# Optimization experiments

Hardware: AMD Instinct MI355X
Metric: run time of the kernel (lower is better)

Reference implementation:

```python
import jax, jax.numpy as jnp
import numpy as np

B, T_ENC, D_IN = 8, 512, 512
T_DEC, ODIM = 150, 80
D_RNN, PRE, ATTN, LOC, K = 1024, 256, 128, 32, 31
ZONEOUT = 0.1


def setup_inputs() -> dict:
    key = jax.random.key(0)
    ks = jax.random.split(key, 24)
    s = 0.02
    n = jax.random.normal
    inp = {
        "memory": n(ks[0], (B, T_ENC, D_IN), jnp.float32),
        "memory_length": jax.random.randint(ks[1], (B,), 256, T_ENC + 1, jnp.int32),
        "targets": n(ks[2], (B, T_DEC, ODIM), jnp.float32),
        # location-sensitive attention params
        "W_mem": n(ks[3], (ATTN, D_IN), jnp.float32) * s,
        "W_q": n(ks[4], (ATTN, D_RNN), jnp.float32) * s,
        "W_loc": n(ks[5], (ATTN, LOC), jnp.float32) * s,
        "loc_filters": n(ks[6], (LOC, 1, K), jnp.float32) * s,
        "attn_v": n(ks[7], (ATTN,), jnp.float32) * s,
        "attn_b": jnp.zeros((ATTN,), jnp.float32),
        # prenet (80 -> 256 -> 256)
        "pre_W1": n(ks[8], (PRE, ODIM), jnp.float32) * s,
        "pre_b1": jnp.zeros((PRE,), jnp.float32),
        "pre_W2": n(ks[9], (PRE, PRE), jnp.float32) * s,
        "pre_b2": jnp.zeros((PRE,), jnp.float32),
        # LSTM layer 0: input = D_IN + PRE
        "Wi0": n(ks[10], (4 * D_RNN, D_IN + PRE), jnp.float32) * s,
        "Wh0": n(ks[11], (4 * D_RNN, D_RNN), jnp.float32) * s,
        "bl0": jnp.zeros((4 * D_RNN,), jnp.float32),
        # LSTM layer 1
        "Wi1": n(ks[12], (4 * D_RNN, D_RNN), jnp.float32) * s,
        "Wh1": n(ks[13], (4 * D_RNN, D_RNN), jnp.float32) * s,
        "bl1": jnp.zeros((4 * D_RNN,), jnp.float32),
        # projections from zcs = [h_last, att_c] of width D_RNN + D_IN
        "feat_W": n(ks[14], (ODIM, D_RNN + D_IN), jnp.float32) * s,
        "stop_W": n(ks[15], (1, D_RNN + D_IN), jnp.float32) * s,
        "stop_b": jnp.zeros((1,), jnp.float32),
    }
    return inp


def _lstm_cell(x, h, c, Wi, Wh, b):
    g = x @ Wi.T + h @ Wh.T + b
    i, f, gc, o = jnp.split(g, 4, axis=-1)  # torch LSTMCell gate order
    c_new = jax.nn.sigmoid(f) * c + jax.nn.sigmoid(i) * jnp.tanh(gc)
    h_new = jax.nn.sigmoid(o) * jnp.tanh(c_new)
    # zoneout (expected value / eval form)
    return (1.0 - ZONEOUT) * h_new + ZONEOUT * h, (1.0 - ZONEOUT) * c_new + ZONEOUT * c


def reference(memory, memory_length, targets, W_mem, W_q, W_loc, loc_filters,
              attn_v, attn_b, pre_W1, pre_b1, pre_W2, pre_b2,
              Wi0, Wh0, bl0, Wi1, Wh1, bl1, feat_W, stop_W, stop_b):
    b, t_enc, _ = memory.shape
    proc_mem = jnp.einsum('btd,ad->bta', memory, W_mem)           # [B,T,ATTN]
    mask = jnp.arange(t_enc)[None, :] < memory_length[:, None]    # [B,T]

    def step(carry, prev_out):
        h0, c0, h1, c1, att_cum = carry
        # location features: conv over cumulative attention weights
        f = jax.lax.conv_general_dilated(att_cum[:, None, :], loc_filters,
                                         (1,), 'SAME')            # [B,LOC,T]
        loc = jnp.einsum('bct,ac->bta', f, W_loc)                  # [B,T,ATTN]
        q = (h0 @ W_q.T)[:, None, :]                               # [B,1,ATTN]
        e = jnp.einsum('a,bta->bt', attn_v,
                       jnp.tanh(proc_mem + loc + q + attn_b))      # [B,T]
        att_w = jax.nn.softmax(jnp.where(mask, e, -1e9), axis=-1)
        att_c = jnp.einsum('bt,btd->bd', att_w, memory)            # [B,D_IN]
        # prenet on previous output (dropout off: deterministic reference)
        p = jax.nn.relu(prev_out @ pre_W1.T + pre_b1)
        p = jax.nn.relu(p @ pre_W2.T + pre_b2)
        x = jnp.concatenate([att_c, p], axis=1)                    # [B,D_IN+PRE]
        h0, c0 = _lstm_cell(x, h0, c0, Wi0, Wh0, bl0)
        h1, c1 = _lstm_cell(h0, h1, c1, Wi1, Wh1, bl1)
        zcs = jnp.concatenate([h1, att_c], axis=1)                 # use_concate=True
        out = zcs @ feat_W.T                                       # [B,ODIM]
        stop = zcs @ stop_W.T + stop_b                             # [B,1]
        return (h0, c0, h1, c1, att_cum + att_w), (out, stop, att_w)

    z = jnp.zeros((b, D_RNN), memory.dtype)
    init = (z, z, z, z, jnp.zeros((b, t_enc), memory.dtype))
    # teacher forcing: prev_out at step t is targets[t-1], zeros at t=0
    prev_outs = jnp.concatenate(
        [jnp.zeros((b, 1, ODIM), targets.dtype), targets[:, :-1]], axis=1)
    _, (outs, stops, att_ws) = jax.lax.scan(step, init,
                                            jnp.swapaxes(prev_outs, 0, 1))
    before_outs = jnp.swapaxes(outs, 0, 1)         # [B,T_dec,ODIM]
    stops = jnp.swapaxes(stops, 0, 1)[..., 0]      # [B,T_dec]
    att_ws = jnp.swapaxes(att_ws, 0, 1)            # [B,T_dec,T_enc]
    return before_outs, stops, att_ws
```

## Files before the change

### kernel.cpp

```cpp
#include <hip/hip_runtime.h>
#include <hip/hip_fp16.h>
#include <cstdint>
#include <cstddef>


#define NB 256
#define NT 512

#define Bz   8
#define TE   512
#define DINz 512
#define TDz  150
#define ODz  80
#define DRz  1024
#define PREz 256
#define ATz  128
#define LOCz 32
#define KFz  31

#define OF_P    0
#define OF_PM   307200
#define OF_Q    831488
#define OF_U    832512
#define OF_CUM  836608
#define OF_ATTC 840704
#define OF_S    848896
#define OF_INVS 848912
#define OF_H0   848928
#define OF_C0   857120
#define OF_H1   865312
#define OF_C1   873504
#define OF_GH0  881696
#define OF_GH1  914464
#define OF_BAR  947232

#define OFF_X0   0
#define OFF_X1   2048
#define OFF_EX   4096
#define OFF_EXG  4352
#define OFF_CW   4608
#define OFF_QS   4736
#define OFF_PART 4864
#define OFF_UU   5376
#define OFF_F    5632
#define OFF_V    9600
#define OFF_WA   9728
#define OFF_WB   22016
#define OFF_WG1  4608
#define OFF_WG2  20992
#define SM_TOTF  38400

#define AG __HIP_MEMORY_SCOPE_AGENT

__device__ __forceinline__ float ldg_sc1(const float* p){
  return __hip_atomic_load(p, __ATOMIC_RELAXED, AG);
}
__device__ __forceinline__ void stg_sc1(float* p, float v){
  __hip_atomic_store(p, v, __ATOMIC_RELAXED, AG);
}
__device__ __forceinline__ float4 ldg4_sc1(const float* p){
  float4 r; r.x=ldg_sc1(p); r.y=ldg_sc1(p+1); r.z=ldg_sc1(p+2); r.w=ldg_sc1(p+3);
  return r;
}
__device__ __forceinline__ float fsig_(float x){ return 1.f/(1.f + __expf(-x)); }
__device__ __forceinline__ float ftanh_(float x){
  x = fminf(10.f, fmaxf(-10.f, x));
  float e = __expf(2.f*x);
  return (e - 1.f) / (e + 1.f);
}

__device__ __forceinline__ void grid_barrier(int* bar){
  asm volatile("s_waitcnt vmcnt(0) lgkmcnt(0)" ::: "memory");
  __syncthreads();
  if (threadIdx.x == 0){
    const int lf = blockIdx.x >> 4;
    int* leaf  = bar + (lf << 5);
    int* root  = bar + 512;
    int* ep    = bar + 1024 + (lf << 5);
    int g = __hip_atomic_load(ep, __ATOMIC_RELAXED, AG);
    int lo = __hip_atomic_fetch_add(leaf, 1, __ATOMIC_RELAXED, AG);
    if ((lo & 15) == 15){
      int ro = __hip_atomic_fetch_add(root, 1, __ATOMIC_RELAXED, AG);
      if ((ro & 15) == 15){
        #pragma unroll
        for (int i=0;i<16;++i)
          __hip_atomic_store(bar + 1024 + (i<<5), g + 1, __ATOMIC_RELAXED, AG);
      }
    }
    while (__hip_atomic_load(ep, __ATOMIC_RELAXED, AG) == g)
      __builtin_amdgcn_s_sleep(1);
  }
  __syncthreads();
}
__device__ __forceinline__ void grid_barrier_heavy(int* bar){
  asm volatile("s_waitcnt vmcnt(0) lgkmcnt(0)" ::: "memory");
  __syncthreads();
  if (threadIdx.x == 0){
    __builtin_amdgcn_fence(__ATOMIC_RELEASE, "agent");
    const int lf = blockIdx.x >> 4;
    int* leaf  = bar + (lf << 5);
    int* root  = bar + 512;
    int* ep    = bar + 1024 + (lf << 5);
    int g = __hip_atomic_load(ep, __ATOMIC_RELAXED, AG);
    int lo = __hip_atomic_fetch_add(leaf, 1, __ATOMIC_RELAXED, AG);
    if ((lo & 15) == 15){
      int ro = __hip_atomic_fetch_add(root, 1, __ATOMIC_RELAXED, AG);
      if ((ro & 15) == 15){
        #pragma unroll
        for (int i=0;i<16;++i)
          __hip_atomic_store(bar + 1024 + (i<<5), g + 1, __ATOMIC_RELAXED, AG);
      }
    }
    while (__hip_atomic_load(ep, __ATOMIC_RELAXED, AG) == g)
      __builtin_amdgcn_s_sleep(1);
    __builtin_amdgcn_fence(__ATOMIC_ACQUIRE, "agent");
  }
  __syncthreads();
}

template<int K, bool GM>
__device__ void load_wtile(float* dstf, const float* __restrict__ W, int base){
  __half* dst = (__half*)dstf;
  constexpr int KV = K >> 2;
  constexpr int NV = 32 * KV;
  for (int idx = threadIdx.x; idx < NV; idx += NT){
    int r = idx / KV;
    int c = (idx - r*KV) << 2;
    int grow = GM ? (((r>>3)<<10) + base + (r&7)) : (base + r);
    float4 w = *(const float4*)(W + (size_t)grow*K + c);
    __half* d = dst + (size_t)r*K + c;
    d[0] = __float2half_rn(w.x);
    d[1] = __float2half_rn(w.y);
    d[2] = __float2half_rn(w.z);
    d[3] = __float2half_rn(w.w);
  }
}

__device__ __forceinline__ float reduce_dot(float* sm, float (&acc)[2][8]){
  const int tid = threadIdx.x;
  const int s = tid & 31, pos = tid >> 5;
  #pragma unroll
  for (int i=0;i<2;++i){
    #pragma unroll
    for (int b=0;b<8;++b){
      float v = acc[i][b];
      v += __shfl_xor(v, 16, 64);
      v += __shfl_xor(v,  8, 64);
      v += __shfl_xor(v,  4, 64);
      v += __shfl_xor(v,  2, 64);
      v += __shfl_xor(v,  1, 64);
      acc[i][b] = v;
    }
  }
  if (s == 0){
    #pragma unroll
    for (int i=0;i<2;++i)
      #pragma unroll
      for (int b=0;b<8;++b)
        sm[OFF_EX + ((((pos<<1)+i)<<3) | b)] = acc[i][b];
  }
  __syncthreads();
  return (tid < 256) ? sm[OFF_EX + tid] : 0.f;
}

template<int K, int XMODE>
__device__ float gemm32x8_lds(float* sm, const __half* __restrict__ wlds,
                              const float* __restrict__ xsrc,
                              const float* __restrict__ attc_cur,
                              const float* __restrict__ S_cur,
                              const float* __restrict__ Pt)
{
  constexpr int NCH = K >> 8;
  const int tid = threadIdx.x;
  const int s = tid & 31, pos = tid >> 5;
  float acc[2][8];
  #pragma unroll
  for (int i=0;i<2;++i)
    #pragma unroll
    for (int b=0;b<8;++b) acc[i][b] = 0.f;

  const int xb = tid >> 6, xcol = (tid & 63) << 2;
  float4 xreg[NCH];
  if constexpr (XMODE == 0){
    #pragma unroll
    for (int ch=0; ch<NCH; ++ch)
      xreg[ch] = ldg4_sc1(xsrc + (size_t)xb*K + (ch<<8) + xcol);
  } else {
    float xsc = 1.f / ldg_sc1(S_cur + xb);
    #pragma unroll
    for (int ch=0; ch<2; ++ch){
      float4 v = ldg4_sc1(attc_cur + (xb<<9) + (ch<<8) + xcol);
      v.x*=xsc; v.y*=xsc; v.z*=xsc; v.w*=xsc;
      xreg[ch] = v;
    }
    xreg[2] = *(const float4*)(Pt + (xb<<8) + xcol);
  }
  *(float4*)&sm[OFF_X0 + (xb<<8) + xcol] = xreg[0];
  __syncthreads();
  #pragma unroll
  for (int ch=0; ch<NCH; ++ch){
    if (ch+1 < NCH)
      *(float4*)&sm[(((ch+1)&1) ? OFF_X1 : OFF_X0) + (xb<<8) + xcol] = xreg[(ch+1 < NCH) ? ch+1 : 0];
    const float* xbase = &sm[((ch&1) ? OFF_X1 : OFF_X0)];
    const __half* wch = wlds + (ch<<8);
    #pragma unroll
    for (int j=0;j<2;++j){
      const int k = (j<<7) + (s<<2);
      float4 xv[8];
      #pragma unroll
      for (int b=0;b<8;++b) xv[b] = *(const float4*)&xbase[(b<<8) + k];
      #pragma unroll
      for (int i=0;i<2;++i){
        const int row = (pos<<1) + i;
        uint2 w2 = *(const uint2*)&wch[(size_t)row*K + k];
        __half2 ha = *reinterpret_cast<const __half2*>(&w2.x);
        __half2 hb = *reinterpret_cast<const __half2*>(&w2.y);
        float2 fa = __half22float2(ha);
        float2 fb = __half22float2(hb);
        #pragma unroll
        for (int b=0;b<8;++b){
          acc[i][b] = fmaf(fa.x, xv[b].x, acc[i][b]);
          acc[i][b] = fmaf(fa.y, xv[b].y, acc[i][b]);
          acc[i][b] = fmaf(fb.x, xv[b].z, acc[i][b]);
          acc[i][b] = fmaf(fb.y, xv[b].w, acc[i][b]);
        }
      }
    }
    __syncthreads();
  }
  return reduce_dot(sm, acc);
}

__device__ float gemm32x8_gw(float* sm, const float* __restrict__ W, int rowbase,
                             const float* __restrict__ xsrc)
{
  const int tid = threadIdx.x;
  const int s = tid & 31, pos = tid >> 5;
  float acc[2][8];
  #pragma unroll
  for (int i=0;i<2;++i)
    #pragma unroll
    for (int b=0;b<8;++b) acc[i][b] = 0.f;
  const int xb = tid >> 6, xcol = (tid & 63) << 2;
  float4 xreg[4];
  #pragma unroll
  for (int ch=0; ch<4; ++ch)
    xreg[ch] = ldg4_sc1(xsrc + (size_t)xb*1024 + (ch<<8) + xcol);
  const float* w0 = W + (size_t)(rowbase + (pos<<1))*1024 + (s<<2);
  *(float4*)&sm[OFF_X0 + (xb<<8) + xcol] = xreg[0];
  __syncthreads();
  #pragma unroll
  for (int ch=0; ch<4; ++ch){
    float4 wr[2][2];
    #pragma unroll
    for (int j=0;j<2;++j)
      #pragma unroll
      for (int i=0;i<2;++i)
        wr[j][i] = *(const float4*)(w0 + (size_t)i*1024 + (ch<<8) + (j<<7));
    if (ch+1 < 4)
      *(float4*)&sm[(((ch+1)&1) ? OFF_X1 : OFF_X0) + (xb<<8) + xcol] = xreg[(ch+1<4)?ch+1:0];
    const float* xbase = &sm[((ch&1) ? OFF_X1 : OFF_X0)];
    #pragma unroll
    for (int j=0;j<2;++j){
      const int k = (j<<7) + (s<<2);
      float4 xv[8];
      #pragma unroll
      for (int b=0;b<8;++b) xv[b] = *(const float4*)&xbase[(b<<8) + k];
      #pragma unroll
      for (int i=0;i<2;++i){
        float4 wv = wr[j][i];
        #pragma unroll
        for (int b=0;b<8;++b){
          acc[i][b] = fmaf(wv.x, xv[b].x, acc[i][b]);
          acc[i][b] = fmaf(wv.y, xv[b].y, acc[i][b]);
          acc[i][b] = fmaf(wv.z, xv[b].z, acc[i][b]);
          acc[i][b] = fmaf(wv.w, xv[b].w, acc[i][b]);
        }
      }
    }
    __syncthreads();
  }
  return reduce_dot(sm, acc);
}

__device__ __forceinline__ float prefetch_gh(const float* gh, int u0){
  const int tid = threadIdx.x;
  if (tid >= 256) return 0.f;
  int row32 = tid >> 3, b = tid & 7;
  int gate = row32 >> 3, ul = row32 & 7;
  return ldg_sc1(&gh[(((gate<<10) + u0 + ul)<<3) + b]);
}
__device__ __forceinline__ float prefetch_h(const float* h, int u0){
  const int tid = threadIdx.x;
  if (tid >= 64) return 0.f;
  return ldg_sc1(&h[((tid&7)<<10) + u0 + (tid>>3)]);
}

__device__ void lstm_epilogue(float* sm, float dot, float ghb,
                              const float* __restrict__ bias, float hold,
                              float* __restrict__ h, float* __restrict__ c, int u0)
{
  const int tid = threadIdx.x;
  if (tid < 256){
    int row32 = tid >> 3;
    int gate = row32 >> 3, ul = row32 & 7;
    sm[OFF_EXG + tid] = dot + bias[(gate<<10) + u0 + ul] + ghb;
  }
  __syncthreads();
  if (tid < 64){
    float gi = sm[OFF_EXG + tid];
    float gf = sm[OFF_EXG + 64 + tid];
    float gg = sm[OFF_EXG + 128 + tid];
    float go = sm[OFF_EXG + 192 + tid];
    int ul2 = tid >> 3, b2 = tid & 7;
    int hi = (b2<<10) + u0 + ul2;
    float co = c[hi];
    float cn = fsig_(gf)*co + fsig_(gi)*ftanh_(gg);
    float hn = fsig_(go)*ftanh_(cn);
    c[hi] = 0.9f*cn + 0.1f*co;
    stg_sc1(&h[hi], 0.9f*hn + 0.1f*hold);
  }
}

__device__ void outstop_wave(int rr, int tp, int par,
    const float* __restrict__ feat_W, const float* __restrict__ stop_W,
    const float* __restrict__ stop_b, const float* __restrict__ h1,
    const float* __restrict__ attc, const float* __restrict__ iSw,
    float* __restrict__ d_out)
{
  if (rr >= 648) return;
  int b = rr / 81, r = rr - 81*b;
  int lane = threadIdx.x & 63;
  const float4* Wr = (const float4*)((r < 80) ? (feat_W + (size_t)r*1536) : stop_W);
  float inv = ldg_sc1(iSw + (par<<3) + b);
  float acc = 0.f, acc2 = 0.f;
  #pragma unroll
  for (int j=0;j<4;++j){
    int p = lane + (j<<6);
    float4 w = Wr[p], x = ldg4_sc1(h1 + (b<<10) + (p<<2));
    acc = fmaf(w.x,x.x, fmaf(w.y,x.y, fmaf(w.z,x.z, fmaf(w.w,x.w, acc))));
  }
  #pragma unroll
  for (int j=4;j<6;++j){
    int p = lane + (j<<6);
    float4 w = Wr[p], x = ldg4_sc1(attc + (par<<12) + (b<<9) + ((p-256)<<2));
    acc2 = fmaf(w.x,x.x, fmaf(w.y,x.y, fmaf(w.z,x.z, fmaf(w.w,x.w, acc2))));
  }
  acc += acc2 * inv;
  acc += __shfl_down(acc, 32, 64);
  acc += __shfl_down(acc, 16, 64);
  acc += __shfl_down(acc,  8, 64);
  acc += __shfl_down(acc,  4, 64);
  acc += __shfl_down(acc,  2, 64);
  acc += __shfl_down(acc,  1, 64);
  if (lane == 0){
    if (r < 80) d_out[((size_t)b*TDz + tp)*ODz + r] = acc;
    else        d_out[96000 + (size_t)b*TDz + tp] = acc + stop_b[0];
  }
}

extern "C" __global__ void __launch_bounds__(NT, 2) dec_kernel(
  const float* __restrict__ memory, const int* __restrict__ mlen, const float* __restrict__ targets,
  const float* __restrict__ W_mem, const float* __restrict__ W_q, const float* __restrict__ W_loc,
  const float* __restrict__ loc_f, const float* __restrict__ attn_v, const float* __restrict__ attn_b,
  const float* __restrict__ pre_W1, const float* __restrict__ pre_b1,
  const float* __restrict__ pre_W2, const float* __restrict__ pre_b2,
  const float* __restrict__ Wi0, const float* __restrict__ Wh0, const float* __restrict__ bl0,
  const float* __restrict__ Wi1, const float* __restrict__ Wh1, const float* __restrict__ bl1,
  const float* __restrict__ feat_W, const float* __restrict__ stop_W, const float* __restrict__ stop_b,
  float* __restrict__ d_out, float* __restrict__ ws)
{
  __shared__ float sm[SM_TOTF];
  const int blk = blockIdx.x, tid = threadIdx.x;

  float* Pw   = ws + OF_P;
  float* pmT  = ws + OF_PM;
  float* qw   = ws + OF_Q;
  float* uw   = ws + OF_U;
  float* cum  = ws + OF_CUM;
  float* attc = ws + OF_ATTC;
  float* Sw   = ws + OF_S;
  float* iSw  = ws + OF_INVS;
  float* h0 = ws + OF_H0; float* c0 = ws + OF_C0;
  float* h1 = ws + OF_H1; float* c1 = ws + OF_C1;
  float* gh0 = ws + OF_GH0; float* gh1 = ws + OF_GH1;
  int* bar = (int*)(ws + OF_BAR);

  const bool is_attn = (blk < 64);
  const int ab  = blk >> 3;
  const int ai0 = (blk & 7) << 6;
  const int il  = tid & 63;
  const int ag  = tid >> 6;

  {
    const int gs = NB*NT;
    const int gid = blk*NT + tid;
    for (int i = gid; i < 98304; i += gs) h0[i] = 0.f;
    for (int i = gid; i < 1024;  i += gs) qw[i]  = 0.f;
    for (int i = gid; i < 4096;  i += gs) cum[i] = 0.f;
    for (int i = gid; i < 8192;  i += gs) attc[i] = 0.f;
    if (gid < 32) Sw[gid] = 0.f;

    if (blk < 124){
      load_wtile<768, true >(&sm[OFF_WA], Wi0, blk<<3);
      load_wtile<1024,false>(&sm[OFF_WB], Wh0, blk<<5);
    } else if (blk < 128){
      load_wtile<768, true >(&sm[OFF_WA], Wi0, blk<<3);
      load_wtile<1024,false>(&sm[OFF_WB], W_q, (blk-124)<<5);
    } else {
      load_wtile<1024,false>(&sm[OFF_WG1], Wh1, (blk-128)<<5);
      load_wtile<1024,true >(&sm[OFF_WG2], Wi1, (blk-128)<<3);
    }

    if (is_attn){
      float pacc[16];
      #pragma unroll
      for (int j=0;j<16;++j) pacc[j] = 0.f;
      for (int dc=0; dc<4; ++dc){
        for (int idx = tid; idx < 8192; idx += NT){
          int r = idx >> 7, d = idx & 127;
          sm[r*129 + d] = memory[(size_t)((ab<<9)+ai0+r)*DINz + (dc<<7) + d];
        }
        __syncthreads();
        #pragma unroll
        for (int j=0;j<16;++j){
          int a = (ag<<4) + j;
          const float* wr = W_mem + (size_t)a*DINz + (dc<<7);
          const float* mr = &sm[il*129];
          float acc = 0.f;
          for (int d=0; d<128; d+=4){
            acc = fmaf(mr[d  ], wr[d  ], acc);
            acc = fmaf(mr[d+1], wr[d+1], acc);
            acc = fmaf(mr[d+2], wr[d+2], acc);
            acc = fmaf(mr[d+3], wr[d+3], acc);
          }
          pacc[j] += acc;
        }
        __syncthreads();
      }
      #pragma unroll
      for (int j=0;j<16;++j){
        int a = (ag<<4) + j;
        pmT[((size_t)blk<<13) + (a<<6) + il] = pacc[j] + attn_b[a];
      }
      for (int idx = tid; idx < ATz*KFz; idx += NT){
        int a = idx / KFz, k = idx - a*KFz;
        float s2 = 0.f;
        #pragma unroll
        for (int c2=0;c2<LOCz;++c2) s2 = fmaf(W_loc[(a<<5)+c2], loc_f[c2*KFz+k], s2);
        sm[OFF_F + idx] = s2;
      }
      if (tid < 128) sm[OFF_V + tid] = attn_v[tid];
      __syncthreads();
    }

    const int th = tid >> 8, t2 = tid & 255, base = th << 9;
    for (int it=0; it<3; ++it){
      int pp = (blk<<1) + th + (it<<9);
      bool act = pp < 1200;
      if (act && t2 < ODz){
        int tt = pp >> 3, bb = pp & 7;
        sm[base + t2] = (tt==0) ? 0.f : targets[((size_t)bb*TDz + (tt-1))*ODz + t2];
      }
      __syncthreads();
      if (act){
        float a1 = pre_b1[t2];
        for (int k=0;k<ODz;++k) a1 = fmaf(pre_W1[t2*ODz+k], sm[base+k], a1);
        sm[base + 128 + t2] = fmaxf(a1, 0.f);
      }
      __syncthreads();
      if (act){
        float a2 = pre_b2[t2];
        for (int k=0;k<PREz;++k) a2 = fmaf(pre_W2[(t2<<8)+k], sm[base+128+k], a2);
        Pw[((size_t)pp<<8) + t2] = fmaxf(a2, 0.f);
      }
      __syncthreads();
    }
  }
  grid_barrier_heavy(bar);

  for (int t = 0; t < TDz; ++t){
    const int cur = t & 1, prv = cur ^ 1;

    if (is_attn){
      if (tid < 94){
        int gi = ai0 - 15 + tid;
        sm[OFF_CW + tid] = (gi >= 0 && gi < TE) ? ldg_sc1(&cum[(ab<<9)+gi]) : 0.f;
      }
      if (tid < 128) sm[OFF_QS + tid] = ldg_sc1(&qw[(tid<<3) + ab]);
      __syncthreads();
      float part = 0.f;
      #pragma unroll
      for (int j=0;j<16;++j){
        int a = (ag<<4) + j;
        const float* fb = &sm[OFF_F + a*KFz];
        float conv = 0.f;
        #pragma unroll
        for (int k=0;k<KFz;++k) conv = fmaf(fb[k], sm[OFF_CW + il + k], conv);
        float pv = pmT[((size_t)blk<<13) + (a<<6) + il];
        part = fmaf(sm[OFF_V + a], ftanh_(pv + sm[OFF_QS + a] + conv), part);
      }
      sm[OFF_PART + (il<<3) + ag] = part;
      __syncthreads();
      if (tid < 64){
        float e = 0.f;
        #pragma unroll
        for (int k=0;k<8;++k) e += sm[OFF_PART + (tid<<3) + k];
        int gi = ai0 + tid;
        float uu = (gi < mlen[ab]) ? __expf(e) : 0.f;
        stg_sc1(&uw[(ab<<9)+gi], uu);
        sm[OFF_UU + tid] = uu;
      }
      __syncthreads();
      if (tid == 0){
        float ssum = 0.f;
        #pragma unroll
        for (int k=0;k<64;++k) ssum += sm[OFF_UU + k];
        atomicAdd(&Sw[(cur<<3)+ab], ssum);
      }
      {
        float acc = 0.f;
        const float* mrow = memory + (size_t)((ab<<9)+ai0)*DINz + tid;
        #pragma unroll 8
        for (int i=0;i<64;++i)
          acc = fmaf(sm[OFF_UU + i], mrow[(size_t)i*DINz], acc);
        atomicAdd(&attc[(cur<<12) + (ab<<9) + tid], acc);
      }
    } else if (blk < 68){
      const int tile = 124 + (blk - 64);
      float dot = gemm32x8_gw(sm, Wh0, tile<<5, h0);
      if (tid < 256) stg_sc1(&gh0[(tile<<8) + tid], dot);
    } else if (blk >= 128){
      const int tile = blk - 128;
      float dot = gemm32x8_lds<1024,0>(sm, (const __half*)&sm[OFF_WG1], h1,
                                       nullptr, nullptr, nullptr);
      if (tid < 256) stg_sc1(&gh1[(tile<<8) + tid], dot);
    }
    grid_barrier(bar);

    if (blk < 128){
      const int u0 = blk << 3;
      float ghb  = prefetch_gh(gh0, u0);
      float hold = prefetch_h(h0, u0);
      float dot = gemm32x8_lds<768,1>(sm, (const __half*)&sm[OFF_WA], nullptr,
                                      attc + (cur<<12), Sw + (cur<<3),
                                      Pw + ((size_t)t<<11));
      lstm_epilogue(sm, dot, ghb, bl0, hold, h0, c0, u0);
    } else if (blk < 136){
      const int b = blk - 128;
      float Sv = __hip_atomic_load(&Sw[(cur<<3)+b], __ATOMIC_RELAXED, AG);
      float inv = 1.f / Sv;
      if (tid == 0) stg_sc1(&iSw[(cur<<3)+b], inv);
      for (int i = tid; i < TE; i += NT){
        float u = ldg_sc1(&uw[(b<<9)+i]);
        float w = u * inv;
        d_out[97200 + ((size_t)b*TDz + t)*TE + i] = w;
        stg_sc1(&cum[(b<<9)+i], ldg_sc1(&cum[(b<<9)+i]) + w);
      }
    } else if (blk < 217){
      if (t > 0)
        outstop_wave((blk-136)*8 + (tid>>6), t-1, prv,
                     feat_W, stop_W, stop_b, h1, attc, iSw, d_out);
    }
    grid_barrier(bar);

    if (blk < 124){
      float dot = gemm32x8_lds<1024,0>(sm, (const __half*)&sm[OFF_WB], h0,
                                       nullptr, nullptr, nullptr);
      if (tid < 256) stg_sc1(&gh0[(blk<<8) + tid], dot);
    } else if (blk < 128){
      const int rt = blk - 124;
      float dot = gemm32x8_lds<1024,0>(sm, (const __half*)&sm[OFF_WB], h0,
                                       nullptr, nullptr, nullptr);
      if (tid < 256) stg_sc1(&qw[(rt<<8) + tid], dot);
      const int zbase = (prv<<12) + (rt<<10);
      for (int i = tid; i < 1024; i += NT) stg_sc1(&attc[zbase + i], 0.f);
      if (rt == 0 && tid < 8) stg_sc1(&Sw[(prv<<3)+tid], 0.f);
    } else {
      const int u0 = (blk - 128) << 3;
      float ghb  = prefetch_gh(gh1, u0);
      float hold = prefetch_h(h1, u0);
      float dot = gemm32x8_lds<1024,0>(sm, (const __half*)&sm[OFF_WG2], h0,
                                       nullptr, nullptr, nullptr);
      lstm_epilogue(sm, dot, ghb, bl1, hold, h1, c1, u0);
    }
    grid_barrier(bar);
  }

  if (blk >= 136 && blk < 217)
    outstop_wave((blk-136)*8 + (tid>>6), TDz-1, 1,
                 feat_W, stop_W, stop_b, h1, attc, iSw, d_out);
}

extern "C" void kernel_launch(void* const* d_in, const int* in_sizes, int n_in,
                              void* d_out, int out_size, void* d_ws, size_t ws_size,
                              hipStream_t stream)
{
  (void)in_sizes; (void)n_in; (void)out_size; (void)ws_size;
  (void)hipMemsetAsync((char*)d_ws + (size_t)OF_BAR*4, 0, 6144, stream);
  dec_kernel<<<dim3(NB), dim3(NT), 0, stream>>>(
    (const float*)d_in[0],  (const int*)d_in[1],   (const float*)d_in[2],
    (const float*)d_in[3],  (const float*)d_in[4],  (const float*)d_in[5],
    (const float*)d_in[6],  (const float*)d_in[7],  (const float*)d_in[8],
    (const float*)d_in[9],  (const float*)d_in[10], (const float*)d_in[11], (const float*)d_in[12],
    (const float*)d_in[13], (const float*)d_in[14], (const float*)d_in[15],
    (const float*)d_in[16], (const float*)d_in[17], (const float*)d_in[18],
    (const float*)d_in[19], (const float*)d_in[20], (const float*)d_in[21],
    (float*)d_out, (float*)d_ws);
}
```

Baseline: 5.674 ms.

## Restructure decoder step into two-phase pipeline with fused LSTM weights in LDS

Reorganizes each decoder step from three grid barriers to two. Layer-1 LSTM now runs one step behind, in parallel with attention, using double-buffered h0/h1/qw/attc. Each block keeps concatenated input and recurrent fp16 weights in LDS, which removes the separate gh precompute pass and the global-weight GEMM. The query projection is folded into the layer-0 epilogue through atomics, and attention is spread over 128 blocks instead of 64. This adds atomic contention on qw and a larger LDS footprint, with occupancy dropping to one block per CU.

```diff
diff --git a/kernel.cpp b/kernel.cpp
--- a/kernel.cpp
+++ b/kernel.cpp
@@ -7,7 +7,6 @@
 #define NB 256
 #define NT 512
 
-#define Bz   8
 #define TE   512
 #define DINz 512
 #define TDz  150
@@ -18,37 +17,34 @@
 #define LOCz 32
 #define KFz  31
 
-#define OF_P    0
-#define OF_PM   307200
-#define OF_Q    831488
-#define OF_U    832512
-#define OF_CUM  836608
-#define OF_ATTC 840704
-#define OF_S    848896
-#define OF_INVS 848912
-#define OF_H0   848928
-#define OF_C0   857120
-#define OF_H1   865312
-#define OF_C1   873504
-#define OF_GH0  881696
-#define OF_GH1  914464
-#define OF_BAR  947232
+#define OF_P     0
+#define OF_PM    307200
+#define OF_Q     831488
+#define OF_U     833536
+#define OF_CUM   837632
+#define OF_ATTC  841728
+#define OF_ATTCN 849920
+#define OF_S     858112
+#define OF_H0    858128
+#define OF_C0    874512
+#define OF_H1    882704
+#define OF_C1    899088
+#define OF_BAR   907280
 
 #define OFF_X0   0
 #define OFF_X1   2048
 #define OFF_EX   4096
 #define OFF_EXG  4352
-#define OFF_CW   4608
-#define OFF_QS   4736
-#define OFF_PART 4864
-#define OFF_UU   5376
-#define OFF_F    5632
-#define OFF_V    9600
-#define OFF_WA   9728
-#define OFF_WB   22016
-#define OFF_WG1  4608
-#define OFF_WG2  20992
-#define SM_TOTF  38400
+#define OFF_HN   4608
+#define OFF_W    4672
+#define OFF_WQT  33344
+#define OFF_F    34368
+#define OFF_V    38336
+#define OFF_CW   38464
+#define OFF_QS   38528
+#define OFF_PART 38656
+#define OFF_UU   39168
+#define SM_TOTF  39200
 
 #define AG __HIP_MEMORY_SCOPE_AGENT
 
@@ -61,6 +57,9 @@
 __device__ __forceinline__ float4 ldg4_sc1(const float* p){
   float4 r; r.x=ldg_sc1(p); r.y=ldg_sc1(p+1); r.z=ldg_sc1(p+2); r.w=ldg_sc1(p+3);
   return r;
+}
+__device__ __forceinline__ void stg4_sc1(float* p, float4 v){
+  stg_sc1(p, v.x); stg_sc1(p+1, v.y); stg_sc1(p+2, v.z); stg_sc1(p+3, v.w);
 }
 __device__ __forceinline__ float fsig_(float x){ return 1.f/(1.f + __expf(-x)); }
 __device__ __forceinline__ float ftanh_(float x){
@@ -118,21 +117,32 @@
   __syncthreads();
 }
 
-template<int K, bool GM>
-__device__ void load_wtile(float* dstf, const float* __restrict__ W, int base){
-  __half* dst = (__half*)dstf;
-  constexpr int KV = K >> 2;
-  constexpr int NV = 32 * KV;
-  for (int idx = threadIdx.x; idx < NV; idx += NT){
-    int r = idx / KV;
-    int c = (idx - r*KV) << 2;
-    int grow = GM ? (((r>>3)<<10) + base + (r&7)) : (base + r);
-    float4 w = *(const float4*)(W + (size_t)grow*K + c);
-    __half* d = dst + (size_t)r*K + c;
-    d[0] = __float2half_rn(w.x);
-    d[1] = __float2half_rn(w.y);
-    d[2] = __float2half_rn(w.z);
-    d[3] = __float2half_rn(w.w);
+__device__ void load_wc0(float* smW, const float* __restrict__ Wi0,
+                         const float* __restrict__ Wh0, int u0){
+  __half* dst = (__half*)smW;
+  for (int idx = threadIdx.x; idx < 32*448; idx += NT){
+    int r = idx / 448, c4 = (idx - r*448) << 2;
+    int grow = ((r>>3)<<10) + u0 + (r&7);
+    const float* src = (c4 < 768) ? (Wi0 + (size_t)grow*768 + c4)
+                                  : (Wh0 + (size_t)grow*1024 + (c4-768));
+    float4 w = *(const float4*)src;
+    __half* d = dst + (size_t)r*1792 + c4;
+    d[0]=__float2half_rn(w.x); d[1]=__float2half_rn(w.y);
+    d[2]=__float2half_rn(w.z); d[3]=__float2half_rn(w.w);
+  }
+}
+__device__ void load_wc1(float* smW, const float* __restrict__ Wi1,
+                         const float* __restrict__ Wh1, int u0){
+  __half* dst = (__half*)smW;
+  for (int idx = threadIdx.x; idx < 32*512; idx += NT){
+    int r = idx >> 9, c4 = (idx & 511) << 2;
+    int grow = ((r>>3)<<10) + u0 + (r&7);
+    const float* src = (c4 < 1024) ? (Wi1 + (size_t)grow*1024 + c4)
+                                   : (Wh1 + (size_t)grow*1024 + (c4-1024));
+    float4 w = *(const float4*)src;
+    __half* d = dst + (size_t)r*2048 + c4;
+    d[0]=__float2half_rn(w.x); d[1]=__float2half_rn(w.y);
+    d[2]=__float2half_rn(w.z); d[3]=__float2half_rn(w.w);
   }
 }
 
@@ -163,44 +173,25 @@
   return (tid < 256) ? sm[OFF_EX + tid] : 0.f;
 }
 
-template<int K, int XMODE>
-__device__ float gemm32x8_lds(float* sm, const __half* __restrict__ wlds,
-                              const float* __restrict__ xsrc,
-                              const float* __restrict__ attc_cur,
-                              const float* __restrict__ S_cur,
-                              const float* __restrict__ Pt)
-{
-  constexpr int NCH = K >> 8;
+template<int NCH>
+__device__ float gemm_core(float* sm, const __half* __restrict__ wlds,
+                           float4 (&xreg)[NCH]){
   const int tid = threadIdx.x;
   const int s = tid & 31, pos = tid >> 5;
+  const int xb = tid >> 6, xcol = (tid & 63) << 2;
+  constexpr int K = NCH << 8;
   float acc[2][8];
   #pragma unroll
   for (int i=0;i<2;++i)
     #pragma unroll
     for (int b=0;b<8;++b) acc[i][b] = 0.f;
-
-  const int xb = tid >> 6, xcol = (tid & 63) << 2;
-  float4 xreg[NCH];
-  if constexpr (XMODE == 0){
-    #pragma unroll
-    for (int ch=0; ch<NCH; ++ch)
-      xreg[ch] = ldg4_sc1(xsrc + (size_t)xb*K + (ch<<8) + xcol);
-  } else {
-    float xsc = 1.f / ldg_sc1(S_cur + xb);
-    #pragma unroll
-    for (int ch=0; ch<2; ++ch){
-      float4 v = ldg4_sc1(attc_cur + (xb<<9) + (ch<<8) + xcol);
-      v.x*=xsc; v.y*=xsc; v.z*=xsc; v.w*=xsc;
-      xreg[ch] = v;
-    }
-    xreg[2] = *(const float4*)(Pt + (xb<<8) + xcol);
-  }
   *(float4*)&sm[OFF_X0 + (xb<<8) + xcol] = xreg[0];
   __syncthreads();
   #pragma unroll
   for (int ch=0; ch<NCH; ++ch){
     if (ch+1 < NCH)
-      *(float4*)&sm[(((ch+1)&1) ? OFF_X1 : OFF_X0) + (xb<<8) + xcol] = xreg[(ch+1 < NCH) ? ch+1 : 0];
+      *(float4*)&sm[(((ch+1)&1) ? OFF_X1 : OFF_X0) + (xb<<8) + xcol] =
+          xreg[(ch+1 < NCH) ? ch+1 : 0];
     const float* xbase = &sm[((ch&1) ? OFF_X1 : OFF_X0)];
     const __half* wch = wlds + (ch<<8);
     #pragma unroll
@@ -231,122 +222,34 @@
   return reduce_dot(sm, acc);
 }
 
-__device__ float gemm32x8_gw(float* sm, const float* __restrict__ W, int rowbase,
-                             const float* __restrict__ xsrc)
-{
-  const int tid = threadIdx.x;
-  const int s = tid & 31, pos = tid >> 5;
-  float acc[2][8];
-  #pragma unroll
-  for (int i=0;i<2;++i)
-    #pragma unroll
-    for (int b=0;b<8;++b) acc[i][b] = 0.f;
-  const int xb = tid >> 6, xcol = (tid & 63) << 2;
-  float4 xreg[4];
-  #pragma unroll
-  for (int ch=0; ch<4; ++ch)
-    xreg[ch] = ldg4_sc1(xsrc + (size_t)xb*1024 + (ch<<8) + xcol);
-  const float* w0 = W + (size_t)(rowbase + (pos<<1))*1024 + (s<<2);
-  *(float4*)&sm[OFF_X0 + (xb<<8) + xcol] = xreg[0];
-  __syncthreads();
-  #pragma unroll
-  for (int ch=0; ch<4; ++ch){
-    float4 wr[2][2];
-    #pragma unroll
-    for (int j=0;j<2;++j)
-      #pragma unroll
-      for (int i=0;i<2;++i)
-        wr[j][i] = *(const float4*)(w0 + (size_t)i*1024 + (ch<<8) + (j<<7));
-    if (ch+1 < 4)
-      *(float4*)&sm[(((ch+1)&1) ? OFF_X1 : OFF_X0) + (xb<<8) + xcol] = xreg[(ch+1<4)?ch+1:0];
-    const float* xbase = &sm[((ch&1) ? OFF_X1 : OFF_X0)];
-    #pragma unroll
-    for (int j=0;j<2;++j){
-      const int k = (j<<7) + (s<<2);
-      float4 xv[8];
-      #pragma unroll
-      for (int b=0;b<8;++b) xv[b] = *(const float4*)&xbase[(b<<8) + k];
-      #pragma unroll
-      for (int i=0;i<2;++i){
-        float4 wv = wr[j][i];
-        #pragma unroll
-        for (int b=0;b<8;++b){
-          acc[i][b] = fmaf(wv.x, xv[b].x, acc[i][b]);
-          acc[i][b] = fmaf(wv.y, xv[b].y, acc[i][b]);
-          acc[i][b] = fmaf(wv.z, xv[b].z, acc[i][b]);
-          acc[i][b] = fmaf(wv.w, xv[b].w, acc[i][b]);
-        }
-      }
-    }
-    __syncthreads();
-  }
-  return reduce_dot(sm, acc);
-}
-
-__device__ __forceinline__ float prefetch_gh(const float* gh, int u0){
-  const int tid = threadIdx.x;
-  if (tid >= 256) return 0.f;
-  int row32 = tid >> 3, b = tid & 7;
-  int gate = row32 >> 3, ul = row32 & 7;
-  return ldg_sc1(&gh[(((gate<<10) + u0 + ul)<<3) + b]);
-}
 __device__ __forceinline__ float prefetch_h(const float* h, int u0){
   const int tid = threadIdx.x;
   if (tid >= 64) return 0.f;
   return ldg_sc1(&h[((tid&7)<<10) + u0 + (tid>>3)]);
 }
 
-__device__ void lstm_epilogue(float* sm, float dot, float ghb,
-                              const float* __restrict__ bias, float hold,
-                              float* __restrict__ h, float* __restrict__ c, int u0)
-{
-  const int tid = threadIdx.x;
-  if (tid < 256){
-    int row32 = tid >> 3;
-    int gate = row32 >> 3, ul = row32 & 7;
-    sm[OFF_EXG + tid] = dot + bias[(gate<<10) + u0 + ul] + ghb;
-  }
-  __syncthreads();
-  if (tid < 64){
-    float gi = sm[OFF_EXG + tid];
-    float gf = sm[OFF_EXG + 64 + tid];
-    float gg = sm[OFF_EXG + 128 + tid];
-    float go = sm[OFF_EXG + 192 + tid];
-    int ul2 = tid >> 3, b2 = tid & 7;
-    int hi = (b2<<10) + u0 + ul2;
-    float co = c[hi];
-    float cn = fsig_(gf)*co + fsig_(gi)*ftanh_(gg);
-    float hn = fsig_(go)*ftanh_(cn);
-    c[hi] = 0.9f*cn + 0.1f*co;
-    stg_sc1(&h[hi], 0.9f*hn + 0.1f*hold);
-  }
-}
-
-__device__ void outstop_wave(int rr, int tp, int par,
+__device__ void outstop_wave(int rr, int tp,
     const float* __restrict__ feat_W, const float* __restrict__ stop_W,
-    const float* __restrict__ stop_b, const float* __restrict__ h1,
-    const float* __restrict__ attc, const float* __restrict__ iSw,
-    float* __restrict__ d_out)
+    const float* __restrict__ stop_b, const float* __restrict__ h1b,
+    const float* __restrict__ attcn, float* __restrict__ d_out)
 {
   if (rr >= 648) return;
   int b = rr / 81, r = rr - 81*b;
   int lane = threadIdx.x & 63;
   const float4* Wr = (const float4*)((r < 80) ? (feat_W + (size_t)r*1536) : stop_W);
-  float inv = ldg_sc1(iSw + (par<<3) + b);
-  float acc = 0.f, acc2 = 0.f;
+  float acc = 0.f;
   #pragma unroll
   for (int j=0;j<4;++j){
     int p = lane + (j<<6);
-    float4 w = Wr[p], x = ldg4_sc1(h1 + (b<<10) + (p<<2));
+    float4 w = Wr[p], x = ldg4_sc1(h1b + (b<<10) + (p<<2));
     acc = fmaf(w.x,x.x, fmaf(w.y,x.y, fmaf(w.z,x.z, fmaf(w.w,x.w, acc))));
   }
   #pragma unroll
   for (int j=4;j<6;++j){
     int p = lane + (j<<6);
-    float4 w = Wr[p], x = ldg4_sc1(attc + (par<<12) + (b<<9) + ((p-256)<<2));
-    acc2 = fmaf(w.x,x.x, fmaf(w.y,x.y, fmaf(w.z,x.z, fmaf(w.w,x.w, acc2))));
-  }
-  acc += acc2 * inv;
+    float4 w = Wr[p], x = ldg4_sc1(attcn + (b<<9) + ((p-256)<<2));
+    acc = fmaf(w.x,x.x, fmaf(w.y,x.y, fmaf(w.z,x.z, fmaf(w.w,x.w, acc))));
+  }
   acc += __shfl_down(acc, 32, 64);
   acc += __shfl_down(acc, 16, 64);
   acc += __shfl_down(acc,  8, 64);
@@ -359,7 +262,7 @@
   }
 }
 
-extern "C" __global__ void __launch_bounds__(NT, 2) dec_kernel(
+extern "C" __global__ void __launch_bounds__(NT, 1) dec_kernel(
   const float* __restrict__ memory, const int* __restrict__ mlen, const float* __restrict__ targets,
   const float* __restrict__ W_mem, const float* __restrict__ W_q, const float* __restrict__ W_loc,
   const float* __restrict__ loc_f, const float* __restrict__ attn_v, const float* __restrict__ attn_b,
@@ -379,52 +282,46 @@
   float* uw   = ws + OF_U;
   float* cum  = ws + OF_CUM;
   float* attc = ws + OF_ATTC;
+  float* attcn= ws + OF_ATTCN;
   float* Sw   = ws + OF_S;
-  float* iSw  = ws + OF_INVS;
   float* h0 = ws + OF_H0; float* c0 = ws + OF_C0;
   float* h1 = ws + OF_H1; float* c1 = ws + OF_C1;
-  float* gh0 = ws + OF_GH0; float* gh1 = ws + OF_GH1;
   int* bar = (int*)(ws + OF_BAR);
 
-  const bool is_attn = (blk < 64);
-  const int ab  = blk >> 3;
-  const int ai0 = (blk & 7) << 6;
-  const int il  = tid & 63;
-  const int ag  = tid >> 6;
+  const bool is_attn = (blk < 128);
+  const int ab  = blk >> 4;
+  const int ai0 = (blk & 15) << 5;
+  const int il  = tid & 31;
+  const int ag  = tid >> 5;
 
   {
     const int gs = NB*NT;
     const int gid = blk*NT + tid;
-    for (int i = gid; i < 98304; i += gs) h0[i] = 0.f;
-    for (int i = gid; i < 1024;  i += gs) qw[i]  = 0.f;
-    for (int i = gid; i < 4096;  i += gs) cum[i] = 0.f;
-    for (int i = gid; i < 8192;  i += gs) attc[i] = 0.f;
-    if (gid < 32) Sw[gid] = 0.f;
-
-    if (blk < 124){
-      load_wtile<768, true >(&sm[OFF_WA], Wi0, blk<<3);
-      load_wtile<1024,false>(&sm[OFF_WB], Wh0, blk<<5);
-    } else if (blk < 128){
-      load_wtile<768, true >(&sm[OFF_WA], Wi0, blk<<3);
-      load_wtile<1024,false>(&sm[OFF_WB], W_q, (blk-124)<<5);
+    for (int i = gid; i < (OF_BAR - OF_Q); i += gs) ws[OF_Q + i] = 0.f;
+
+    if (is_attn){
+      load_wc0(&sm[OFF_W], Wi0, Wh0, blk<<3);
+      for (int i = tid; i < 1024; i += NT){
+        int u = i >> 7, a = i & 127;
+        sm[OFF_WQT + i] = W_q[((size_t)a<<10) + (blk<<3) + u];
+      }
     } else {
-      load_wtile<1024,false>(&sm[OFF_WG1], Wh1, (blk-128)<<5);
-      load_wtile<1024,true >(&sm[OFF_WG2], Wi1, (blk-128)<<3);
+      load_wc1(&sm[OFF_W], Wi1, Wh1, (blk-128)<<3);
     }
 
     if (is_attn){
-      float pacc[16];
-      #pragma unroll
-      for (int j=0;j<16;++j) pacc[j] = 0.f;
+      float pacc[8];
+      #pragma unroll
+      for (int j=0;j<8;++j) pacc[j] = 0.f;
       for (int dc=0; dc<4; ++dc){
-        for (int idx = tid; idx < 8192; idx += NT){
+        for (int idx = tid; idx < 4096; idx += NT){
           int r = idx >> 7, d = idx & 127;
           sm[r*129 + d] = memory[(size_t)((ab<<9)+ai0+r)*DINz + (dc<<7) + d];
         }
         __syncthreads();
         #pragma unroll
-        for (int j=0;j<16;++j){
-          int a = (ag<<4) + j;
+        for (int j=0;j<8;++j){
+          int a = (ag<<3) + j;
           const float* wr = W_mem + (size_t)a*DINz + (dc<<7);
           const float* mr = &sm[il*129];
           float acc = 0.f;
@@ -439,9 +336,9 @@
         __syncthreads();
       }
       #pragma unroll
-      for (int j=0;j<16;++j){
-        int a = (ag<<4) + j;
-        pmT[((size_t)blk<<13) + (a<<6) + il] = pacc[j] + attn_b[a];
+      for (int j=0;j<8;++j){
+        int a = (ag<<3) + j;
+        pmT[((size_t)blk<<12) + (a<<5) + il] = pacc[j] + attn_b[a];
       }
       for (int idx = tid; idx < ATz*KFz; idx += NT){
         int a = idx / KFz, k = idx - a*KFz;
@@ -456,10 +353,10 @@
 
     const int th = tid >> 8, t2 = tid & 255, base = th << 9;
     for (int it=0; it<3; ++it){
-      int pp = (blk<<1) + th + (it<<9);
-      bool act = pp < 1200;
+      int pp2 = (blk<<1) + th + (it<<9);
+      bool act = pp2 < 1200;
       if (act && t2 < ODz){
-        int tt = pp >> 3, bb = pp & 7;
+        int tt = pp2 >> 3, bb = pp2 & 7;
         sm[base + t2] = (tt==0) ? 0.f : targets[((size_t)bb*TDz + (tt-1))*ODz + t2];
       }
       __syncthreads();
@@ -472,7 +369,7 @@
       if (act){
         float a2 = pre_b2[t2];
         for (int k=0;k<PREz;++k) a2 = fmaf(pre_W2[(t2<<8)+k], sm[base+128+k], a2);
-        Pw[((size_t)pp<<8) + t2] = fmaxf(a2, 0.f);
+        Pw[((size_t)pp2<<8) + t2] = fmaxf(a2, 0.f);
       }
       __syncthreads();
     }
@@ -480,32 +377,32 @@
   grid_barrier_heavy(bar);
 
   for (int t = 0; t < TDz; ++t){
-    const int cur = t & 1, prv = cur ^ 1;
+    const int p = t & 1, pp = p ^ 1;
 
     if (is_attn){
-      if (tid < 94){
+      if (tid < 62){
         int gi = ai0 - 15 + tid;
         sm[OFF_CW + tid] = (gi >= 0 && gi < TE) ? ldg_sc1(&cum[(ab<<9)+gi]) : 0.f;
       }
-      if (tid < 128) sm[OFF_QS + tid] = ldg_sc1(&qw[(tid<<3) + ab]);
+      if (tid < 128) sm[OFF_QS + tid] = ldg_sc1(&qw[(p<<10) + (tid<<3) + ab]);
       __syncthreads();
       float part = 0.f;
       #pragma unroll
-      for (int j=0;j<16;++j){
-        int a = (ag<<4) + j;
+      for (int j=0;j<8;++j){
+        int a = (ag<<3) + j;
         const float* fb = &sm[OFF_F + a*KFz];
         float conv = 0.f;
         #pragma unroll
         for (int k=0;k<KFz;++k) conv = fmaf(fb[k], sm[OFF_CW + il + k], conv);
-        float pv = pmT[((size_t)blk<<13) + (a<<6) + il];
+        float pv = pmT[((size_t)blk<<12) + (a<<5) + il];
         part = fmaf(sm[OFF_V + a], ftanh_(pv + sm[OFF_QS + a] + conv), part);
       }
-      sm[OFF_PART + (il<<3) + ag] = part;
-      __syncthreads();
-      if (tid < 64){
+      sm[OFF_PART + (il<<4) + ag] = part;
+      __syncthreads();
+      if (tid < 32){
         float e = 0.f;
         #pragma unroll
-        for (int k=0;k<8;++k) e += sm[OFF_PART + (tid<<3) + k];
+        for (int k=0;k<16;++k) e += sm[OFF_PART + (tid<<4) + k];
         int gi = ai0 + tid;
         float uu = (gi < mlen[ab]) ? __expf(e) : 0.f;
         stg_sc1(&uw[(ab<<9)+gi], uu);
@@ -515,42 +412,113 @@
       if (tid == 0){
         float ssum = 0.f;
         #pragma unroll
-        for (int k=0;k<64;++k) ssum += sm[OFF_UU + k];
-        atomicAdd(&Sw[(cur<<3)+ab], ssum);
+        for (int k=0;k<32;++k) ssum += sm[OFF_UU + k];
+        atomicAdd(&Sw[(p<<3)+ab], ssum);
       }
       {
         float acc = 0.f;
         const float* mrow = memory + (size_t)((ab<<9)+ai0)*DINz + tid;
         #pragma unroll 8
-        for (int i=0;i<64;++i)
+        for (int i=0;i<32;++i)
           acc = fmaf(sm[OFF_UU + i], mrow[(size_t)i*DINz], acc);
-        atomicAdd(&attc[(cur<<12) + (ab<<9) + tid], acc);
-      }
-    } else if (blk < 68){
-      const int tile = 124 + (blk - 64);
-      float dot = gemm32x8_gw(sm, Wh0, tile<<5, h0);
-      if (tid < 256) stg_sc1(&gh0[(tile<<8) + tid], dot);
-    } else if (blk >= 128){
-      const int tile = blk - 128;
-      float dot = gemm32x8_lds<1024,0>(sm, (const __half*)&sm[OFF_WG1], h1,
-                                       nullptr, nullptr, nullptr);
-      if (tid < 256) stg_sc1(&gh1[(tile<<8) + tid], dot);
+        atomicAdd(&attc[(p<<12) + (ab<<9) + tid], acc);
+      }
+    } else {
+      if (blk == 128 && tid < 8) stg_sc1(&Sw[(pp<<3)+tid], 0.f);
+      if (t > 0){
+        const int u0 = (blk - 128) << 3;
+        const float* h0pp = h0 + (pp<<13);
+        const float* h1p  = h1 + (p<<13);
+        const int xb = tid >> 6, xcol = (tid & 63) << 2;
+        float hold = prefetch_h(h1p, u0);
+        float4 xr[8];
+        #pragma unroll
+        for (int c=0;c<4;++c) xr[c]   = ldg4_sc1(h0pp + (xb<<10) + (c<<8) + xcol);
+        #pragma unroll
+        for (int c=0;c<4;++c) xr[4+c] = ldg4_sc1(h1p  + (xb<<10) + (c<<8) + xcol);
+        float dot = gemm_core<8>(sm, (const __half*)&sm[OFF_W], xr);
+        if (tid < 256){
+          int row32 = tid >> 3, gate = row32 >> 3, ul = row32 & 7;
+          sm[OFF_EXG + tid] = dot + bl1[(gate<<10) + u0 + ul];
+        }
+        __syncthreads();
+        if (tid < 64){
+          float gi = sm[OFF_EXG + tid];
+          float gf = sm[OFF_EXG + 64 + tid];
+          float gg = sm[OFF_EXG + 128 + tid];
+          float go = sm[OFF_EXG + 192 + tid];
+          int ul2 = tid >> 3, b2 = tid & 7;
+          int hi = (b2<<10) + u0 + ul2;
+          float co = c1[hi];
+          float cn = fsig_(gf)*co + fsig_(gi)*ftanh_(gg);
+          float hn = fsig_(go)*ftanh_(cn);
+          c1[hi] = 0.9f*cn + 0.1f*co;
+          stg_sc1(h1 + (pp<<13) + hi, 0.9f*hn + 0.1f*hold);
+        }
+      }
     }
     grid_barrier(bar);
 
-    if (blk < 128){
+    if (is_attn){
       const int u0 = blk << 3;
-      float ghb  = prefetch_gh(gh0, u0);
-      float hold = prefetch_h(h0, u0);
-      float dot = gemm32x8_lds<768,1>(sm, (const __half*)&sm[OFF_WA], nullptr,
-                                      attc + (cur<<12), Sw + (cur<<3),
-                                      Pw + ((size_t)t<<11));
-      lstm_epilogue(sm, dot, ghb, bl0, hold, h0, c0, u0);
+      const int xb = tid >> 6, xcol = (tid & 63) << 2;
+      float* attc_p = attc + (p<<12);
+      const float* h0pp = h0 + (pp<<13);
+      float sv = ldg_sc1(Sw + (p<<3) + xb);
+      float hold = prefetch_h(h0pp, u0);
+      float4 xr[7];
+      xr[0] = ldg4_sc1(attc_p + (xb<<9) + xcol);
+      xr[1] = ldg4_sc1(attc_p + (xb<<9) + 256 + xcol);
+      xr[2] = *(const float4*)(Pw + ((size_t)t<<11) + (xb<<8) + xcol);
+      #pragma unroll
+      for (int c=0;c<4;++c) xr[3+c] = ldg4_sc1(h0pp + (xb<<10) + (c<<8) + xcol);
+      float inv = 1.f / sv;
+      xr[0].x*=inv; xr[0].y*=inv; xr[0].z*=inv; xr[0].w*=inv;
+      xr[1].x*=inv; xr[1].y*=inv; xr[1].z*=inv; xr[1].w*=inv;
+      if (blk == 0){
+        float* an = attcn + (p<<12) + (xb<<9) + xcol;
+        stg4_sc1(an, xr[0]);
+        stg4_sc1(an + 256, xr[1]);
+      }
+      float dot = gemm_core<7>(sm, (const __half*)&sm[OFF_W], xr);
+      if (tid < 256){
+        int row32 = tid >> 3, gate = row32 >> 3, ul = row32 & 7;
+        sm[OFF_EXG + tid] = dot + bl0[(gate<<10) + u0 + ul];
+      }
+      __syncthreads();
+      if (tid < 64){
+        float gi = sm[OFF_EXG + tid];
+        float gf = sm[OFF_EXG + 64 + tid];
+        float gg = sm[OFF_EXG + 128 + tid];
+        float go = sm[OFF_EXG + 192 + tid];
+        int ul2 = tid >> 3, b2 = tid & 7;
+        int hi = (b2<<10) + u0 + ul2;
+        float co = c0[hi];
+        float cn = fsig_(gf)*co + fsig_(gi)*ftanh_(gg);
+        float hn = fsig_(go)*ftanh_(cn);
+        c0[hi] = 0.9f*cn + 0.1f*co;
+        float hz = 0.9f*hn + 0.1f*hold;
+        stg_sc1(h0 + (p<<13) + hi, hz);
+        sm[OFF_HN + (b2<<3) + ul2] = hz;
+      }
+      __syncthreads();
+      {
+        int a = tid >> 3, b = tid & 7;
+        float v0 = 0.f, v1 = 0.f;
+        #pragma unroll
+        for (int u=0;u<8;++u){
+          float hu = sm[OFF_HN + (b<<3) + u];
+          v0 = fmaf(sm[OFF_WQT + (u<<7) + a     ], hu, v0);
+          v1 = fmaf(sm[OFF_WQT + (u<<7) + a + 64], hu, v1);
+        }
+        float* qdst = qw + (pp<<10);
+        atomicAdd(qdst + (a<<3) + b, v0);
+        atomicAdd(qdst + ((a+64)<<3) + b, v1);
+      }
     } else if (blk < 136){
       const int b = blk - 128;
-      float Sv = __hip_atomic_load(&Sw[(cur<<3)+b], __ATOMIC_RELAXED, AG);
+      float Sv = __hip_atomic_load(&Sw[(p<<3)+b], __ATOMIC_RELAXED, AG);
       float inv = 1.f / Sv;
-      if (tid == 0) stg_sc1(&iSw[(cur<<3)+b], inv);
       for (int i = tid; i < TE; i += NT){
         float u = ldg_sc1(&uw[(b<<9)+i]);
         float w = u * inv;
@@ -559,37 +527,50 @@
       }
     } else if (blk < 217){
       if (t > 0)
-        outstop_wave((blk-136)*8 + (tid>>6), t-1, prv,
-                     feat_W, stop_W, stop_b, h1, attc, iSw, d_out);
+        outstop_wave((blk-136)*8 + (tid>>6), t-1,
+                     feat_W, stop_W, stop_b, h1 + (pp<<13), attcn + (pp<<12), d_out);
+    } else if (blk < 225){
+      stg_sc1(&attc[(pp<<12) + ((blk-217)<<9) + tid], 0.f);
+    } else if (blk < 227){
+      stg_sc1(&qw[(p<<10) + ((blk-225)<<9) + tid], 0.f);
     }
     grid_barrier(bar);
-
-    if (blk < 124){
-      float dot = gemm32x8_lds<1024,0>(sm, (const __half*)&sm[OFF_WB], h0,
-                                       nullptr, nullptr, nullptr);
-      if (tid < 256) stg_sc1(&gh0[(blk<<8) + tid], dot);
-    } else if (blk < 128){
-      const int rt = blk - 124;
-      float dot = gemm32x8_lds<1024,0>(sm, (const __half*)&sm[OFF_WB], h0,
-                                       nullptr, nullptr, nullptr);
-      if (tid < 256) stg_sc1(&qw[(rt<<8) + tid], dot);
-      const int zbase = (prv<<12) + (rt<<10);
-      for (int i = tid; i < 1024; i += NT) stg_sc1(&attc[zbase + i], 0.f);
-      if (rt == 0 && tid < 8) stg_sc1(&Sw[(prv<<3)+tid], 0.f);
-    } else {
-      const int u0 = (blk - 128) << 3;
-      float ghb  = prefetch_gh(gh1, u0);
-      float hold = prefetch_h(h1, u0);
-      float dot = gemm32x8_lds<1024,0>(sm, (const __half*)&sm[OFF_WG2], h0,
-                                       nullptr, nullptr, nullptr);
-      lstm_epilogue(sm, dot, ghb, bl1, hold, h1, c1, u0);
-    }
-    grid_barrier(bar);
-  }
-
+  }
+
+  if (!is_attn){
+    const int u0 = (blk - 128) << 3;
+    const float* h0pp = h0 + (1<<13);
+    const float* h1p  = h1 + (0<<13);
+    const int xb = tid >> 6, xcol = (tid & 63) << 2;
+    float hold = prefetch_h(h1p, u0);
+    float4 xr[8];
+    #pragma unroll
+    for (int c=0;c<4;++c) xr[c]   = ldg4_sc1(h0pp + (xb<<10) + (c<<8) + xcol);
+    #pragma unroll
+    for (int c=0;c<4;++c) xr[4+c] = ldg4_sc1(h1p  + (xb<<10) + (c<<8) + xcol);
+    float dot = gemm_core<8>(sm, (const __half*)&sm[OFF_W], xr);
+    if (tid < 256){
+      int row32 = tid >> 3, gate = row32 >> 3, ul = row32 & 7;
+      sm[OFF_EXG + tid] = dot + bl1[(gate<<10) + u0 + ul];
+    }
+    __syncthreads();
+    if (tid < 64){
+      float gi = sm[OFF_EXG + tid];
+      float gf = sm[OFF_EXG + 64 + tid];
+      float gg = sm[OFF_EXG + 128 + tid];
+      float go = sm[OFF_EXG + 192 + tid];
+      int ul2 = tid >> 3, b2 = tid & 7;
+      int hi = (b2<<10) + u0 + ul2;
+      float co = c1[hi];
+      float cn = fsig_(gf)*co + fsig_(gi)*ftanh_(gg);
+      float hn = fsig_(go)*ftanh_(cn);
+      stg_sc1(h1 + (1<<13) + hi, 0.9f*hn + 0.1f*hold);
+    }
+  }
+  grid_barrier(bar);
   if (blk >= 136 && blk < 217)
-    outstop_wave((blk-136)*8 + (tid>>6), TDz-1, 1,
-                 feat_W, stop_W, stop_b, h1, attc, iSw, d_out);
+    outstop_wave((blk-136)*8 + (tid>>6), TDz-1,
+                 feat_W, stop_W, stop_b, h1 + (1<<13), attcn + (1<<12), d_out);
 }
 
 extern "C" void kernel_launch(void* const* d_in, const int* in_sizes, int n_in,
```

Result: slower. 9.984 ms (+75.9%).
